# Kernel optimization log

Hardware: AMD Instinct MI355X
Metric: run time of the kernel (lower is better)

Reference implementation:

```python
import jax, jax.numpy as jnp
import numpy as np
from functools import partial

# ---- NASA Li-ion battery default parameters (Daigle model) ----
P = {}
P['qMobile'] = 7600.0
P['xnMax'] = 0.6; P['xnMin'] = 0.0
P['xpMax'] = 1.0; P['xpMin'] = 0.4
P['qmax'] = P['qMobile'] / (P['xnMax'] - P['xnMin'])  # 12666.667
P['Ro'] = 0.117215
P['R'] = 8.3144621
P['F'] = 96487.0
P['alpha'] = 0.5
P['Sn'] = 0.000437545
P['Sp'] = 0.00030962
P['kn'] = 2120.96
P['kp'] = 248898.0
P['Volume'] = 2e-5
P['VolumeSurf'] = 0.1
P['tDiffusion'] = 7e6
P['to'] = 6.08671
P['tsn'] = 1001.38
P['tsp'] = 46.4311
P['VolS'] = P['VolumeSurf'] * P['Volume']
P['VolB'] = P['Volume'] - P['VolS']
P['qSMax'] = P['qmax'] * P['VolS'] / P['Volume']
P['qBMax'] = P['qmax'] * P['VolB'] / P['Volume']
U0P, U0N = 4.03, 0.01
APS = np.array([-31593.7, 0.106747, 24606.4, -78561.9, 13317.9, 307387.0,
                84916.1, -1.07469e6, 2285.04, 990894.0, 283920.0, -161513.0,
                -469218.0], dtype=np.float32)
ANS = np.array([86.19], dtype=np.float32)
DT = 1.0
B, T = 2048, 1024


def _vint(x, As, F):
    N = As.shape[0]
    k = jnp.arange(N, dtype=x.dtype)          # [N]
    ki = jnp.arange(N)
    b = (2.0 * x - 1.0)[..., None]            # [B,1]
    ab, sg = jnp.abs(b), jnp.sign(b)
    # integer-exponent pow with correct sign for negative base
    p_kp1 = ab ** (k + 1.0) * jnp.where((ki + 1) % 2 == 1, sg, 1.0)
    p_km1 = ab ** (k - 1.0) * jnp.where((ki - 1) % 2 != 0, sg, 1.0)
    term = p_kp1 - (2.0 * x * (1.0 - x))[..., None] * k * p_km1
    return (term @ As) / F


def _vint_safe(x, As, F):
    ok = x != 0.5
    sx = jnp.where(ok, x, 1.0)
    return jnp.where(ok, _vint(sx, As, F), 0.0)


def _step(state, i, Aps, Ans):
    tb, Vo, Vsn, Vsp, qnB, qnS, qpB, qpS = state
    R, F, alpha = P['R'], P['F'], P['alpha']
    xpS = qpS / P['qSMax']
    xnS = qnS / P['qSMax']
    Jn0 = P['kn'] * (1.0 - xnS) ** alpha * xnS ** alpha
    Jp0 = P['kp'] * (1.0 - xpS) ** alpha * xpS ** alpha
    dBSn = (qnB / P['VolB'] - qnS / P['VolS']) / P['tDiffusion']
    dBSp = (qpB / P['VolB'] - qpS / P['VolS']) / P['tDiffusion']
    Jn, Jp = i / P['Sn'], i / P['Sp']
    VoN = i * P['Ro']
    VsnN = R * tb / (F * alpha) * jnp.arcsinh(Jn / (2.0 * Jn0))
    VspN = R * tb / (F * alpha) * jnp.arcsinh(Jp / (2.0 * Jp0))
    Ven = U0N + R * tb / F * jnp.log((1.0 - xnS) / xnS) + _vint_safe(xnS, Ans, F)
    Vep = U0P + R * tb / F * jnp.log((1.0 - xpS) / xpS) + _vint_safe(xpS, Aps, F)
    v = Vep - Ven - Vo - Vsn - Vsp
    new = (tb,
           Vo + DT * (VoN - Vo) / P['to'],
           Vsn + DT * (VsnN - Vsn) / P['tsn'],
           Vsp + DT * (VspN - Vsp) / P['tsp'],
           qnB - DT * dBSn,
           qnS + DT * (dBSn - i),
           qpB - DT * dBSp,
           qpS + DT * (i + dBSp))
    return new, v


def setup_inputs() -> dict:
    key = jax.random.key(0)
    k1, = jax.random.split(key, 1)
    i = 0.1 + 0.9 * jax.random.uniform(k1, (B, T), dtype=jnp.float32)  # amps
    qnS0 = P['xnMax'] * P['qmax'] * P['VolS'] / P['Volume']
    qnB0 = P['xnMax'] * P['qmax'] * P['VolB'] / P['Volume']
    qpS0 = P['xpMin'] * P['qmax'] * P['VolS'] / P['Volume']
    qpB0 = P['xpMin'] * P['qmax'] * P['VolB'] / P['Volume']
    x0 = jnp.tile(jnp.array([292.1, 0.0, 0.0, 0.0, qnB0, qnS0, qpB0, qpS0],
                            dtype=jnp.float32), (B, 1))
    return {'i': i, 'x0': x0, 'Aps': jnp.asarray(APS), 'Ans': jnp.asarray(ANS)}


def reference(i, x0, Aps, Ans):
    state0 = tuple(x0[:, j] for j in range(8))
    def body(st, it):
        return _step(st, it, Aps, Ans)
    _, v = jax.lax.scan(body, state0, i.T)  # v: [T,B]
    return v.T  # voltage per cell per step, [B,T]
```

## Files before the change

kernel.cpp:

```cpp
#include <hip/hip_runtime.h>
#include <math.h>


constexpr int NTHR = 256;
constexpr int L = 4;

__global__ __launch_bounds__(NTHR) void battery_scan(
    const float* __restrict__ I, const float* __restrict__ X0,
    const float* __restrict__ Aps, const float* __restrict__ Ans,
    float* __restrict__ out, int Tn)
{
    const int cell = blockIdx.x;
    const int tid  = threadIdx.x;

    __shared__ float sh0[NTHR], sh1[NTHR], sh2[NTHR];

    const float ivB    = (float)(1.0/1.8e-5);
    const float ivS    = (float)(1.0/2.0e-6);
    const float invSum = (float)(1.0/(1.0/1.8e-5 + 1.0/2.0e-6));
    const float aq     = (float)(1.0 - (1.0/1.8e-5 + 1.0/2.0e-6)/7.0e6);
    const float ao     = (float)(1.0 - 1.0/6.08671);
    const float asn    = (float)(1.0 - 1.0/1001.38);
    const float asp    = (float)(1.0 - 1.0/46.4311);
    const float inv_qS = (float)(1.0/1266.6666666666667);
    const float invF   = (float)(1.0/96487.0);
    const float kn     = 2120.96f, kp = 248898.0f;
    const float invSnH = (float)(0.5/0.000437545);
    const float invSpH = (float)(0.5/0.00030962);
    const float Ro_to  = (float)(0.117215/6.08671);
    const float inv_tsn= (float)(1.0/1001.38);
    const float inv_tsp= (float)(1.0/46.4311);
    const float U0P = 4.03f, U0N = 0.01f;

    const float aqp[4]  = {1.f, aq,  aq*aq,   aq*aq*aq};
    const float aop[4]  = {1.f, ao,  ao*ao,   ao*ao*ao};
    const float asnp[4] = {1.f, asn, asn*asn, asn*asn*asn};
    const float aspp[4] = {1.f, asp, asp*asp, asp*asp*asp};
    const float aq4 = aqp[3]*aq, ao4 = aop[3]*ao;
    const float asn4 = asnp[3]*asn, asp4 = aspp[3]*asp;

    const float tb   = X0[cell*8+0];
    const float Vo0  = X0[cell*8+1];
    const float Vsn0 = X0[cell*8+2];
    const float Vsp0 = X0[cell*8+3];
    const float qnB0 = X0[cell*8+4];
    const float qnS0 = X0[cell*8+5];
    const float qpB0 = X0[cell*8+6];
    const float qpS0 = X0[cell*8+7];

    const float rtf  = 8.3144621f * tb * invF;
    const float rtfa = 2.f*rtf;
    const float u_n0 = qnB0 + qnS0;
    const float u_p0 = qpB0 + qpS0;
    const float w_n0 = qnB0*ivB - qnS0*ivS;
    const float w_p0 = qpB0*ivB - qpS0*ivS;
    const float An0  = Ans[0];

    const float t4 = (float)(tid*L);
    const float paq_base  = exp2f(t4 * __log2f(aq));
    const float pao_base  = exp2f(t4 * __log2f(ao));
    const float pasn_base = exp2f(t4 * __log2f(asn));
    const float pasp_base = exp2f(t4 * __log2f(asp));

    const float4 iv4 = *(const float4*)(I + (size_t)cell*Tn + tid*L);
    const float i4[4] = {iv4.x, iv4.y, iv4.z, iv4.w};

    float es[4], eg[4], eo[4];
    {
        float as_=0.f, ag=0.f, aoc=0.f;
        #pragma unroll
        for (int k=0;k<L;++k){
            es[k]=as_; eg[k]=ag; eo[k]=aoc;
            float b = i4[k];
            as_ += b;
            ag  = aq*ag  + b;
            aoc = ao*aoc + b;
        }
        sh0[tid]=as_; sh1[tid]=ag; sh2[tid]=aoc;
    }
    __syncthreads();
    {
        float vs = sh0[tid], vg = sh1[tid], vo = sh2[tid];
        float Rg = aq4, Rr = ao4;
        for (int s=1; s<NTHR; s<<=1){
            float ps=0.f,pg=0.f,po=0.f;
            if (tid>=s){ ps=sh0[tid-s]; pg=sh1[tid-s]; po=sh2[tid-s]; }
            __syncthreads();
            vs += ps; vg += Rg*pg; vo += Rr*po;
            Rg*=Rg; Rr*=Rr;
            sh0[tid]=vs; sh1[tid]=vg; sh2[tid]=vo;
            __syncthreads();
        }
    }
    float cs=0.f, cg=0.f, co=0.f;
    if (tid>0){ cs=sh0[tid-1]; cg=sh1[tid-1]; co=sh2[tid-1]; }

    float vpart[4], bsn[4], bsp[4];
    #pragma unroll
    for (int k=0;k<L;++k){
        float s_t = cs + es[k];
        float g_t = aqp[k]*cg + eg[k];
        float o_t = aop[k]*co + eo[k];
        float u_n = u_n0 - s_t, u_p = u_p0 + s_t;
        float paq = paq_base*aqp[k];
        float w_n = paq*w_n0 + ivS*g_t;
        float w_p = paq*w_p0 - ivS*g_t;
        float qnS = (u_n*ivB - w_n)*invSum;
        float qpS = (u_p*ivB - w_p)*invSum;
        float xnS = qnS*inv_qS, xpS = qpS*inv_qS;
        float Vo_t = (pao_base*aop[k])*Vo0 + Ro_to*o_t;
        float it = i4[k];
        float Jn0 = kn*sqrtf(xnS*(1.f-xnS));
        float Jp0 = kp*sqrtf(xpS*(1.f-xpS));
        float zn = __fdividef(it*invSnH, Jn0);
        float zp = __fdividef(it*invSpH, Jp0);
        float VsnN = rtfa*__logf(zn + sqrtf(__builtin_fmaf(zn,zn,1.f)));
        float VspN = rtfa*__logf(zp + sqrtf(__builtin_fmaf(zp,zp,1.f)));
        float bn_ = 2.f*xnS - 1.f;
        float vint_n = (xnS != 0.5f) ? An0*bn_*invF : 0.f;
        float Ven = U0N + rtf*__logf(__fdividef(1.f-xnS, xnS)) + vint_n;
        float bp_ = 2.f*xpS - 1.f;
        float P1 = Aps[12];
        #pragma unroll
        for (int j=11;j>=0;--j) P1 = P1*bp_ + Aps[j];
        float P2 = 12.f*Aps[12];
        #pragma unroll
        for (int j=11;j>=1;--j) P2 = P2*bp_ + (float)j*Aps[j];
        float vint_p = (xpS != 0.5f)
                     ? (bp_*P1 - 2.f*xpS*(1.f-xpS)*P2)*invF : 0.f;
        float Vep = U0P + rtf*__logf(__fdividef(1.f-xpS, xpS)) + vint_p;
        vpart[k] = Vep - Ven - Vo_t;
        bsn[k] = VsnN * inv_tsn;
        bsp[k] = VspN * inv_tsp;
    }

    float esn[4], esp[4];
    {
        float an=0.f, apv=0.f;
        #pragma unroll
        for (int k=0;k<L;++k){
            esn[k]=an; esp[k]=apv;
            an  = asn*an  + bsn[k];
            apv = asp*apv + bsp[k];
        }
        __syncthreads();
        sh0[tid]=an; sh1[tid]=apv;
    }
    __syncthreads();
    {
        float vn = sh0[tid], vp = sh1[tid];
        float Rn = asn4, Rp = asp4;
        for (int s=1; s<NTHR; s<<=1){
            float pn=0.f, pp=0.f;
            if (tid>=s){ pn=sh0[tid-s]; pp=sh1[tid-s]; }
            __syncthreads();
            vn += Rn*pn; vp += Rp*pp;
            Rn*=Rn; Rp*=Rp;
            sh0[tid]=vn; sh1[tid]=vp;
            __syncthreads();
        }
    }
    float csn=0.f, csp=0.f;
    if (tid>0){ csn=sh0[tid-1]; csp=sh1[tid-1]; }

    float res[4];
    #pragma unroll
    for (int k=0;k<L;++k){
        float Vsn_t = (pasn_base*asnp[k])*Vsn0 + (asnp[k]*csn + esn[k]);
        float Vsp_t = (pasp_base*aspp[k])*Vsp0 + (aspp[k]*csp + esp[k]);
        res[k] = vpart[k] - Vsn_t - Vsp_t;
    }
    *(float4*)(out + (size_t)cell*Tn + tid*L) = make_float4(res[0],res[1],res[2],res[3]);
}

extern "C" void kernel_launch(void* const* d_in, const int* in_sizes, int n_in,
                              void* d_out, int out_size, void* d_ws, size_t ws_size,
                              hipStream_t stream) {
    const float* I   = (const float*)d_in[0];
    const float* X0  = (const float*)d_in[1];
    const float* Aps = (const float*)d_in[2];
    const float* Ans = (const float*)d_in[3];
    float* out = (float*)d_out;

    int Bn = in_sizes[1] / 8;
    int Tn = in_sizes[0] / Bn;

    battery_scan<<<dim3(Bn), dim3(NTHR), 0, stream>>>(I, X0, Aps, Ans, out, Tn);
}
```

Before: 79.23 us.

## Replace shared-memory block scans with wavefront shuffle scans plus cross-wave combine

Swaps the 8-step shared-memory Hillis-Steele scans, each step fenced by two __syncthreads, for intra-wave __shfl_up scans followed by a small cross-wave combine through shared memory, leaving one barrier per scan phase. It also folds the electrode log terms into a single log, uses rsqrt for the exchange current, merges the polynomial and derivative Horner loops, and sets a minimum-blocks launch bound. The goal is to cut barrier and LDS traffic. The risks are a few leftover dead loops and small floating-point differences from the reassociated arithmetic.

```diff
diff --git a/kernel.cpp b/kernel.cpp
--- a/kernel.cpp
+++ b/kernel.cpp
@@ -4,16 +4,20 @@
 
 constexpr int NTHR = 256;
 constexpr int L = 4;
-
-__global__ __launch_bounds__(NTHR) void battery_scan(
+constexpr int NW = NTHR / 64;
+
+__global__ __launch_bounds__(NTHR, 6) void battery_scan2(
     const float* __restrict__ I, const float* __restrict__ X0,
     const float* __restrict__ Aps, const float* __restrict__ Ans,
     float* __restrict__ out, int Tn)
 {
     const int cell = blockIdx.x;
     const int tid  = threadIdx.x;
-
-    __shared__ float sh0[NTHR], sh1[NTHR], sh2[NTHR];
+    const int lane = tid & 63;
+    const int wv   = tid >> 6;
+
+    __shared__ float shA[3][NW];
+    __shared__ float shC[2][NW];
 
     const float ivB    = (float)(1.0/1.8e-5);
     const float ivS    = (float)(1.0/2.0e-6);
@@ -24,13 +28,12 @@
     const float asp    = (float)(1.0 - 1.0/46.4311);
     const float inv_qS = (float)(1.0/1266.6666666666667);
     const float invF   = (float)(1.0/96487.0);
-    const float kn     = 2120.96f, kp = 248898.0f;
-    const float invSnH = (float)(0.5/0.000437545);
-    const float invSpH = (float)(0.5/0.00030962);
+    const float c_zn   = (float)(0.5/0.000437545/2120.96);
+    const float c_zp   = (float)(0.5/0.00030962/248898.0);
     const float Ro_to  = (float)(0.117215/6.08671);
     const float inv_tsn= (float)(1.0/1001.38);
     const float inv_tsp= (float)(1.0/46.4311);
-    const float U0P = 4.03f, U0N = 0.01f;
+    const float U0PN   = 4.03f - 0.01f;
 
     const float aqp[4]  = {1.f, aq,  aq*aq,   aq*aq*aq};
     const float aop[4]  = {1.f, ao,  ao*ao,   ao*ao*ao};
@@ -47,6 +50,7 @@
     const float qnS0 = X0[cell*8+5];
     const float qpB0 = X0[cell*8+6];
     const float qpS0 = X0[cell*8+7];
+    const float An0  = Ans[0];
 
     const float rtf  = 8.3144621f * tb * invF;
     const float rtfa = 2.f*rtf;
@@ -54,121 +58,152 @@
     const float u_p0 = qpB0 + qpS0;
     const float w_n0 = qnB0*ivB - qnS0*ivS;
     const float w_p0 = qpB0*ivB - qpS0*ivS;
-    const float An0  = Ans[0];
-
-    const float t4 = (float)(tid*L);
-    const float paq_base  = exp2f(t4 * __log2f(aq));
-    const float pao_base  = exp2f(t4 * __log2f(ao));
-    const float pasn_base = exp2f(t4 * __log2f(asn));
-    const float pasp_base = exp2f(t4 * __log2f(asp));
+
+    const float fl = (float)lane;
+    const float plq  = exp2f(fl * __log2f(aq4));
+    const float plo  = exp2f(fl * __log2f(ao4));
+    const float pln  = exp2f(fl * __log2f(asn4));
+    const float plp  = exp2f(fl * __log2f(asp4));
 
     const float4 iv4 = *(const float4*)(I + (size_t)cell*Tn + tid*L);
     const float i4[4] = {iv4.x, iv4.y, iv4.z, iv4.w};
 
+    auto wscan = [&](float tot, float R4, float& ep, float& Tw, float& R64) {
+        float v = tot, r = R4;
+        #pragma unroll
+        for (int s = 1; s < 64; s <<= 1) {
+            float p = __shfl_up(v, s);
+            v = (lane >= s) ? fmaf(r, p, v) : v;
+            r *= r;
+        }
+        float e = __shfl_up(v, 1);
+        ep = (lane == 0) ? 0.f : e;
+        Tw = __shfl(v, 63);
+        R64 = r;
+    };
+
     float es[4], eg[4], eo[4];
+    float ts = 0.f, tg = 0.f, to_ = 0.f;
+    #pragma unroll
+    for (int k = 0; k < L; ++k) {
+        es[k] = ts; eg[k] = tg; eo[k] = to_;
+        float b = i4[k];
+        ts  += b;
+        tg   = fmaf(aq, tg, b);
+        to_  = fmaf(ao, to_, b);
+    }
+    float epS, TwS, RS, epG, TwG, RG, epO, TwO, RO;
+    wscan(ts,  1.f, epS, TwS, RS);
+    wscan(tg,  aq4, epG, TwG, RG);
+    wscan(to_, ao4, epO, TwO, RO);
+    if (lane == 0) { shA[0][wv] = TwS; shA[1][wv] = TwG; shA[2][wv] = TwO; }
+    __syncthreads();
+    float Cs = 0.f, Cg = 0.f, Co = 0.f;
+    for (int w2 = 0; w2 < wv; ++w2) {
+        Cs = Cs + shA[0][w2];
+        Cg = fmaf(RG, Cg, 0.f) ; Cg = Cg;
+        Co = Co;
+        (void)0;
+    }
+    Cs = 0.f; Cg = 0.f; Co = 0.f;
+    for (int w2 = 0; w2 < wv; ++w2) {
+        Cs = Cs + shA[0][w2];
+        Cg = fmaf(Cg, RG, shA[1][w2]) - Cg*RG + Cg*RG;
+        Co = Co*RO + shA[2][w2];
+    }
     {
-        float as_=0.f, ag=0.f, aoc=0.f;
+        Cs = 0.f; Cg = 0.f; Co = 0.f;
         #pragma unroll
-        for (int k=0;k<L;++k){
-            es[k]=as_; eg[k]=ag; eo[k]=aoc;
-            float b = i4[k];
-            as_ += b;
-            ag  = aq*ag  + b;
-            aoc = ao*aoc + b;
-        }
-        sh0[tid]=as_; sh1[tid]=ag; sh2[tid]=aoc;
-    }
-    __syncthreads();
-    {
-        float vs = sh0[tid], vg = sh1[tid], vo = sh2[tid];
-        float Rg = aq4, Rr = ao4;
-        for (int s=1; s<NTHR; s<<=1){
-            float ps=0.f,pg=0.f,po=0.f;
-            if (tid>=s){ ps=sh0[tid-s]; pg=sh1[tid-s]; po=sh2[tid-s]; }
-            __syncthreads();
-            vs += ps; vg += Rg*pg; vo += Rr*po;
-            Rg*=Rg; Rr*=Rr;
-            sh0[tid]=vs; sh1[tid]=vg; sh2[tid]=vo;
-            __syncthreads();
-        }
-    }
-    float cs=0.f, cg=0.f, co=0.f;
-    if (tid>0){ cs=sh0[tid-1]; cg=sh1[tid-1]; co=sh2[tid-1]; }
+        for (int w2 = 0; w2 < NW; ++w2) {
+            if (w2 < wv) {
+                Cs = Cs + shA[0][w2];
+                Cg = Cg*RG + shA[1][w2];
+                Co = Co*RO + shA[2][w2];
+            }
+        }
+    }
+    const float cs = epS + Cs;
+    const float cg = fmaf(plq, Cg, epG);
+    const float co = fmaf(plo, Co, epO);
+
+    float pwq = plq, pwo = plo;
+    for (int w2 = 0; w2 < wv; ++w2) { pwq *= RG; pwo *= RO; }
 
     float vpart[4], bsn[4], bsp[4];
-    #pragma unroll
-    for (int k=0;k<L;++k){
+    float tn_ = 0.f, tp_ = 0.f;
+    #pragma unroll
+    for (int k = 0; k < L; ++k) {
         float s_t = cs + es[k];
-        float g_t = aqp[k]*cg + eg[k];
-        float o_t = aop[k]*co + eo[k];
+        float g_t = fmaf(aqp[k], cg, eg[k]);
+        float o_t = fmaf(aop[k], co, eo[k]);
         float u_n = u_n0 - s_t, u_p = u_p0 + s_t;
-        float paq = paq_base*aqp[k];
-        float w_n = paq*w_n0 + ivS*g_t;
-        float w_p = paq*w_p0 - ivS*g_t;
+        float paq = pwq * aqp[k];
+        float w_n = fmaf(paq, w_n0,  ivS*g_t);
+        float w_p = fmaf(paq, w_p0, -ivS*g_t);
         float qnS = (u_n*ivB - w_n)*invSum;
         float qpS = (u_p*ivB - w_p)*invSum;
         float xnS = qnS*inv_qS, xpS = qpS*inv_qS;
-        float Vo_t = (pao_base*aop[k])*Vo0 + Ro_to*o_t;
+        float Vo_t = fmaf(pwo*aop[k], Vo0, Ro_to*o_t);
         float it = i4[k];
-        float Jn0 = kn*sqrtf(xnS*(1.f-xnS));
-        float Jp0 = kp*sqrtf(xpS*(1.f-xpS));
-        float zn = __fdividef(it*invSnH, Jn0);
-        float zp = __fdividef(it*invSpH, Jp0);
-        float VsnN = rtfa*__logf(zn + sqrtf(__builtin_fmaf(zn,zn,1.f)));
-        float VspN = rtfa*__logf(zp + sqrtf(__builtin_fmaf(zp,zp,1.f)));
+
+        float pn = xnS*(1.f - xnS);
+        float pp = xpS*(1.f - xpS);
+        float zn = it * c_zn * rsqrtf(pn);
+        float zp = it * c_zp * rsqrtf(pp);
+        float VsnN = rtfa*__logf(zn + sqrtf(fmaf(zn, zn, 1.f)));
+        float VspN = rtfa*__logf(zp + sqrtf(fmaf(zp, zp, 1.f)));
+
+        float num = (1.f - xpS)*xnS;
+        float den = xpS*(1.f - xnS);
+        float lr  = __logf(__fdividef(num, den));
+
+        float bp_ = 2.f*xpS - 1.f;
+        float P = 0.f, D = 0.f;
+        #pragma unroll
+        for (int j = 12; j >= 0; --j) {
+            D = fmaf(D, bp_, P);
+            P = fmaf(P, bp_, Aps[j]);
+        }
+        float vint_p = (xpS != 0.5f)
+                     ? (bp_*P - 2.f*xpS*(1.f - xpS)*D)*invF : 0.f;
         float bn_ = 2.f*xnS - 1.f;
         float vint_n = (xnS != 0.5f) ? An0*bn_*invF : 0.f;
-        float Ven = U0N + rtf*__logf(__fdividef(1.f-xnS, xnS)) + vint_n;
-        float bp_ = 2.f*xpS - 1.f;
-        float P1 = Aps[12];
-        #pragma unroll
-        for (int j=11;j>=0;--j) P1 = P1*bp_ + Aps[j];
-        float P2 = 12.f*Aps[12];
-        #pragma unroll
-        for (int j=11;j>=1;--j) P2 = P2*bp_ + (float)j*Aps[j];
-        float vint_p = (xpS != 0.5f)
-                     ? (bp_*P1 - 2.f*xpS*(1.f-xpS)*P2)*invF : 0.f;
-        float Vep = U0P + rtf*__logf(__fdividef(1.f-xpS, xpS)) + vint_p;
-        vpart[k] = Vep - Ven - Vo_t;
-        bsn[k] = VsnN * inv_tsn;
-        bsp[k] = VspN * inv_tsp;
-    }
-
-    float esn[4], esp[4];
-    {
-        float an=0.f, apv=0.f;
-        #pragma unroll
-        for (int k=0;k<L;++k){
-            esn[k]=an; esp[k]=apv;
-            an  = asn*an  + bsn[k];
-            apv = asp*apv + bsp[k];
-        }
-        __syncthreads();
-        sh0[tid]=an; sh1[tid]=apv;
-    }
+
+        vpart[k] = U0PN + rtf*lr + vint_p - vint_n - Vo_t;
+        float bn = VsnN * inv_tsn;
+        float bpv = VspN * inv_tsp;
+        bsn[k] = bn; bsp[k] = bpv;
+        tn_ = fmaf(asn, tn_, bn);
+        tp_ = fmaf(asp, tp_, bpv);
+    }
+
+    float epN, TwN, RN, epP, TwP, RP;
+    wscan(tn_, asn4, epN, TwN, RN);
+    wscan(tp_, asp4, epP, TwP, RP);
+    if (lane == 0) { shC[0][wv] = TwN; shC[1][wv] = TwP; }
     __syncthreads();
-    {
-        float vn = sh0[tid], vp = sh1[tid];
-        float Rn = asn4, Rp = asp4;
-        for (int s=1; s<NTHR; s<<=1){
-            float pn=0.f, pp=0.f;
-            if (tid>=s){ pn=sh0[tid-s]; pp=sh1[tid-s]; }
-            __syncthreads();
-            vn += Rn*pn; vp += Rp*pp;
-            Rn*=Rn; Rp*=Rp;
-            sh0[tid]=vn; sh1[tid]=vp;
-            __syncthreads();
-        }
-    }
-    float csn=0.f, csp=0.f;
-    if (tid>0){ csn=sh0[tid-1]; csp=sh1[tid-1]; }
+    float Cn = 0.f, Cp = 0.f;
+    #pragma unroll
+    for (int w2 = 0; w2 < NW; ++w2) {
+        if (w2 < wv) {
+            Cn = Cn*RN + shC[0][w2];
+            Cp = Cp*RP + shC[1][w2];
+        }
+    }
+    const float csn = fmaf(pln, Cn, epN);
+    const float csp = fmaf(plp, Cp, epP);
+    float pwn = pln, pwp = plp;
+    for (int w2 = 0; w2 < wv; ++w2) { pwn *= RN; pwp *= RP; }
 
     float res[4];
-    #pragma unroll
-    for (int k=0;k<L;++k){
-        float Vsn_t = (pasn_base*asnp[k])*Vsn0 + (asnp[k]*csn + esn[k]);
-        float Vsp_t = (pasp_base*aspp[k])*Vsp0 + (aspp[k]*csp + esp[k]);
+    float an_ = 0.f, ap_ = 0.f;
+    #pragma unroll
+    for (int k = 0; k < L; ++k) {
+        float Vsn_t = fmaf(pwn*asnp[k], Vsn0, fmaf(asnp[k], csn, an_));
+        float Vsp_t = fmaf(pwp*aspp[k], Vsp0, fmaf(aspp[k], csp, ap_));
         res[k] = vpart[k] - Vsn_t - Vsp_t;
+        an_ = fmaf(asn, an_, bsn[k]);
+        ap_ = fmaf(asp, ap_, bsp[k]);
     }
     *(float4*)(out + (size_t)cell*Tn + tid*L) = make_float4(res[0],res[1],res[2],res[3]);
 }
@@ -185,5 +220,5 @@
     int Bn = in_sizes[1] / 8;
     int Tn = in_sizes[0] / Bn;
 
-    battery_scan<<<dim3(Bn), dim3(NTHR), 0, stream>>>(I, X0, Aps, Ans, out, Tn);
+    battery_scan2<<<dim3(Bn), dim3(NTHR), 0, stream>>>(I, X0, Aps, Ans, out, Tn);
 }
```

New measurement: 74.66 us. 1.06x faster.
